# Kernel optimization log

Hardware: AMD Instinct MI355X
Metric: run time of the kernel (lower is better)

The kernel has to match this reference:

```python
import jax, jax.numpy as jnp
import numpy as np

MUL0, MUL1, MUL2, NMOD = 128, 64, 32, 2  # multiplicities of 0e,1e,2e and modalities
D0, D1, D2 = MUL0, MUL1 * 3, MUL2 * 5     # 128, 192, 160 -> total 480


def setup_inputs() -> dict:
    key = jax.random.key(0)
    ks = jax.random.split(key, 7)
    N, G = 200000, 512
    x = jax.random.normal(ks[0], (N, D0 + D1 + D2), dtype=jnp.float32)
    modal_attr = jax.random.uniform(ks[1], (G, NMOD), dtype=jnp.float32)
    W0 = jax.random.normal(ks[2], (MUL0, MUL0), dtype=jnp.float32)
    W0m = jax.random.normal(ks[3], (NMOD, MUL0), dtype=jnp.float32)
    W1 = jax.random.normal(ks[4], (MUL1, MUL1), dtype=jnp.float32)
    W2 = jax.random.normal(ks[5], (MUL2, MUL2), dtype=jnp.float32)
    batch = jnp.sort(jax.random.randint(ks[6], (N,), 0, G, dtype=jnp.int64))
    return {"x": x, "modal_attr": modal_attr, "W0": W0, "W0m": W0m,
            "W1": W1, "W2": W2, "batch": batch}


def reference(x, modal_attr, W0, W0m, W1, W2, batch):
    N = x.shape[0]
    # modality one-hot gathered per node and concatenated (appended 2x0e irrep)
    modal = modal_attr[batch]  # [N, NMOD]
    x0 = x[:, :D0]                                   # [N, 128]  0e
    x1 = x[:, D0:D0 + D1].reshape(N, MUL1, 3)        # [N, 64, 3] 1e
    x2 = x[:, D0 + D1:].reshape(N, MUL2, 5)          # [N, 32, 5] 2e
    # e3nn Linear: per-(l,p) block linear, paths summed, /sqrt(total fan-in mul)
    inv0 = 1.0 / np.sqrt(MUL0 + NMOD).astype(np.float32)
    out0 = (x0 @ W0 + modal @ W0m) * inv0            # [N, 128]
    out1 = jnp.einsum('nim,io->nom', x1, W1) * (1.0 / np.sqrt(MUL1).astype(np.float32))
    out2 = jnp.einsum('nim,io->nom', x2, W2) * (1.0 / np.sqrt(MUL2).astype(np.float32))
    return jnp.concatenate([out0, out1.reshape(N, D1), out2.reshape(N, D2)], axis=1)
```

## Files before the change

kernel.cpp:

```cpp
#include <hip/hip_runtime.h>
#include <hip/hip_bf16.h>


typedef __attribute__((ext_vector_type(8))) short  short8;
typedef __attribute__((ext_vector_type(4))) float  f32x4;

#define NTH 256
#define BR  32

#define W0H 0
#define W0L 16384
#define W1H 32768
#define W1L 36864
#define W2H 40960
#define W2L 41984

__device__ __forceinline__ unsigned bc2(__hip_bfloat162 h) {
    unsigned u; __builtin_memcpy(&u, &h, 4); return u;
}

struct HL4 { uint2 h, l; };

__device__ __forceinline__ HL4 split4(float a, float b, float c, float d) {
    __hip_bfloat162 h01 = __float22bfloat162_rn({a, b});
    __hip_bfloat162 h23 = __float22bfloat162_rn({c, d});
    float ra = a - __low2float(h01),  rb = b - __high2float(h01);
    float rc = c - __low2float(h23),  rd = d - __high2float(h23);
    __hip_bfloat162 l01 = __float22bfloat162_rn({ra, rb});
    __hip_bfloat162 l23 = __float22bfloat162_rn({rc, rd});
    HL4 r;
    r.h = make_uint2(bc2(h01), bc2(h23));
    r.l = make_uint2(bc2(l01), bc2(l23));
    return r;
}

__device__ __forceinline__ void split_w(float v, unsigned short& h, unsigned short& l) {
    __hip_bfloat16 hb = __float2bfloat16(v);
    float r = v - __bfloat162float(hb);
    __hip_bfloat16 lb = __float2bfloat16(r);
    __builtin_memcpy(&h, &hb, 2);
    __builtin_memcpy(&l, &lb, 2);
}

__global__ void prep_weights(const float* __restrict__ W0,
                             const float* __restrict__ W1,
                             const float* __restrict__ W2,
                             unsigned short* __restrict__ ws) {
    const int s0     = blockIdx.x * blockDim.x + threadIdx.x;
    const int STRIDE = gridDim.x * blockDim.x;
    for (int s = s0; s < 16384; s += STRIDE) {
        int j = s & 7, l = (s >> 3) & 63, kt = (s >> 9) & 3, ct = s >> 11;
        int col = ct * 16 + (l & 15);
        int k   = kt * 32 + (l >> 4) * 8 + j;
        unsigned short h, lo;
        split_w(W0[k * 128 + col], h, lo);
        ws[W0H + s] = h; ws[W0L + s] = lo;
    }
    for (int s = s0; s < 4096; s += STRIDE) {
        int j = s & 7, l = (s >> 3) & 63, kt = (s >> 9) & 1, ct = s >> 10;
        int col = ct * 16 + (l & 15);
        int k   = kt * 32 + (l >> 4) * 8 + j;
        unsigned short h, lo;
        split_w(W1[k * 64 + col], h, lo);
        ws[W1H + s] = h; ws[W1L + s] = lo;
    }
    for (int s = s0; s < 1024; s += STRIDE) {
        int j = s & 7, l = (s >> 3) & 63, ct = s >> 9;
        int col = ct * 16 + (l & 15);
        int k   = (l >> 4) * 8 + j;
        unsigned short h, lo;
        split_w(W2[k * 32 + col], h, lo);
        ws[W2H + s] = h; ws[W2L + s] = lo;
    }
}

#define MFMA(a, b, c) __builtin_amdgcn_mfma_f32_16x16x32_bf16((a), (b), (c), 0, 0, 0)

__global__ __launch_bounds__(NTH, 4) void irreps_mfma_kernel(
    const float* __restrict__ x,
    const float* __restrict__ modal_attr,
    const float* __restrict__ W0m,
    const unsigned short* __restrict__ wsf,
    const int*   __restrict__ batch,
    float*       __restrict__ out,
    int N)
{
    __shared__ __align__(16) char ldsb[25088];
    float* ldsf = reinterpret_cast<float*>(ldsb);

    const int tid  = threadIdx.x;
    const int w    = tid >> 6;
    const int l    = tid & 63;
    const int r    = l & 15;
    const int kg   = l >> 4;
    const int rb0  = (w >> 1) * 16;
    const int ch   = w & 1;
    const int row0 = blockIdx.x * BR;
    const int arow = rb0 + r;

    float am0[4], am1[4];
    #pragma unroll
    for (int reg = 0; reg < 4; ++reg) {
        int n  = row0 + rb0 + kg * 4 + reg;
        int nc = n < N ? n : N - 1;
        int g  = batch[nc];
        am0[reg] = modal_attr[2 * g];
        am1[reg] = modal_attr[2 * g + 1];
    }

    const float4* __restrict__ x4 = reinterpret_cast<const float4*>(x);

    {
        const int seg = tid & 15;
        const int rr0 = tid >> 4;
        #pragma unroll
        for (int t2 = 0; t2 < 2; ++t2) {
            int rr = rr0 + 16 * t2;
            int n  = row0 + rr; n = n < N ? n : N - 1;
            const float4* src = &x4[(size_t)n * 120 + seg * 2];
            float4 a = src[0], b = src[1];
            HL4 p = split4(a.x, a.y, a.z, a.w);
            HL4 q = split4(b.x, b.y, b.z, b.w);
            int byte = (rr * 256 + seg * 16) ^ ((rr & 7) << 4);
            *reinterpret_cast<uint4*>(ldsb + byte)        = make_uint4(p.h.x, p.h.y, q.h.x, q.h.y);
            *reinterpret_cast<uint4*>(ldsb + 8192 + byte) = make_uint4(p.l.x, p.l.y, q.l.x, q.l.y);
        }
    }
    __syncthreads();

    {
        const int sw = (arow & 7) << 4;
        short8 ah[4], al[4];
        #pragma unroll
        for (int kt = 0; kt < 4; ++kt) {
            int byte = (arow * 256 + kt * 64 + kg * 16) ^ sw;
            ah[kt] = *reinterpret_cast<const short8*>(ldsb + byte);
            al[kt] = *reinterpret_cast<const short8*>(ldsb + 8192 + byte);
        }
        __syncthreads();

        #pragma unroll
        for (int ci = 0; ci < 4; ++ci) {
            int ct = ch * 4 + ci;
            f32x4 acc = {0.f, 0.f, 0.f, 0.f};
            #pragma unroll
            for (int kt = 0; kt < 4; ++kt) {
                int b = ct * 4 + kt;
                short8 bh = *reinterpret_cast<const short8*>(wsf + W0H + (size_t)(b * 64 + l) * 8);
                short8 bl = *reinterpret_cast<const short8*>(wsf + W0L + (size_t)(b * 64 + l) * 8);
                acc = MFMA(ah[kt], bh, acc);
                acc = MFMA(al[kt], bh, acc);
                acc = MFMA(ah[kt], bl, acc);
            }
            int col = ct * 16 + r;
            float wm0 = W0m[col], wm1 = W0m[128 + col];
            #pragma unroll
            for (int reg = 0; reg < 4; ++reg)
                ldsf[(rb0 + kg * 4 + reg) * 132 + col] =
                    (acc[reg] + am0[reg] * wm0 + am1[reg] * wm1) * 0.08770580193070293f;
        }
    }
    __syncthreads();

    {
        #pragma unroll
        for (int j = 0; j < 4; ++j) {
            int idx = tid + j * NTH;
            int row = idx >> 5, c4 = idx & 31;
            int n   = row0 + row;
            if (n < N)
                *reinterpret_cast<float4*>(out + (size_t)n * 480 + c4 * 4) =
                    *reinterpret_cast<const float4*>(ldsf + row * 132 + c4 * 4);
        }
    }
    __syncthreads();

    {
        const int ig  = tid & 15;
        const int rr0 = tid >> 4;
        #pragma unroll
        for (int t2 = 0; t2 < 2; ++t2) {
            int rr = rr0 + 16 * t2;
            int n  = row0 + rr; n = n < N ? n : N - 1;
            const float4* src = &x4[(size_t)n * 120 + 32 + ig * 3];
            float4 f0 = src[0], f1 = src[1], f2 = src[2];
            HL4 s0 = split4(f0.x, f0.w, f1.z, f2.y);
            HL4 s1 = split4(f0.y, f1.x, f1.w, f2.z);
            HL4 s2 = split4(f0.z, f1.y, f2.x, f2.w);
            int rbyte = (rr * 128 + ig * 8) ^ ((rr & 7) << 4);
            *reinterpret_cast<uint2*>(ldsb + 0 * 4096 + rbyte)         = s0.h;
            *reinterpret_cast<uint2*>(ldsb + 1 * 4096 + rbyte)         = s1.h;
            *reinterpret_cast<uint2*>(ldsb + 2 * 4096 + rbyte)         = s2.h;
            *reinterpret_cast<uint2*>(ldsb + 12288 + 0 * 4096 + rbyte) = s0.l;
            *reinterpret_cast<uint2*>(ldsb + 12288 + 1 * 4096 + rbyte) = s1.l;
            *reinterpret_cast<uint2*>(ldsb + 12288 + 2 * 4096 + rbyte) = s2.l;
        }
    }
    __syncthreads();

    {
        const int sw = (arow & 7) << 4;
        short8 ah1[3][2], al1[3][2];
        #pragma unroll
        for (int m = 0; m < 3; ++m) {
            #pragma unroll
            for (int kt = 0; kt < 2; ++kt) {
                int byte = (arow * 128 + kt * 64 + kg * 16) ^ sw;
                ah1[m][kt] = *reinterpret_cast<const short8*>(ldsb + m * 4096 + byte);
                al1[m][kt] = *reinterpret_cast<const short8*>(ldsb + 12288 + m * 4096 + byte);
            }
        }
        __syncthreads();

        #pragma unroll
        for (int ci = 0; ci < 2; ++ci) {
            int ct = ch * 2 + ci;
            short8 bh[2], bl[2];
            #pragma unroll
            for (int kt = 0; kt < 2; ++kt) {
                int b = ct * 2 + kt;
                bh[kt] = *reinterpret_cast<const short8*>(wsf + W1H + (size_t)(b * 64 + l) * 8);
                bl[kt] = *reinterpret_cast<const short8*>(wsf + W1L + (size_t)(b * 64 + l) * 8);
            }
            #pragma unroll
            for (int m = 0; m < 3; ++m) {
                f32x4 acc = {0.f, 0.f, 0.f, 0.f};
                #pragma unroll
                for (int kt = 0; kt < 2; ++kt) {
                    acc = MFMA(ah1[m][kt], bh[kt], acc);
                    acc = MFMA(al1[m][kt], bh[kt], acc);
                    acc = MFMA(ah1[m][kt], bl[kt], acc);
                }
                int col = 3 * (ct * 16 + r) + m;
                #pragma unroll
                for (int reg = 0; reg < 4; ++reg)
                    ldsf[(rb0 + kg * 4 + reg) * 196 + col] = acc[reg] * 0.125f;
            }
        }
    }
    __syncthreads();

    {
        #pragma unroll
        for (int j = 0; j < 6; ++j) {
            int idx = tid + j * NTH;
            int row = idx / 48, c4 = idx - row * 48;
            int n   = row0 + row;
            if (n < N)
                *reinterpret_cast<float4*>(out + (size_t)n * 480 + 128 + c4 * 4) =
                    *reinterpret_cast<const float4*>(ldsf + row * 196 + c4 * 4);
        }
    }
    __syncthreads();

    {
        int rr = tid >> 3, ig = tid & 7;
        int n  = row0 + rr; n = n < N ? n : N - 1;
        const float4* src = &x4[(size_t)n * 120 + 80 + ig * 5];
        float f[20];
        #pragma unroll
        for (int q = 0; q < 5; ++q) {
            float4 v = src[q];
            f[q * 4 + 0] = v.x; f[q * 4 + 1] = v.y; f[q * 4 + 2] = v.z; f[q * 4 + 3] = v.w;
        }
        int rbyte = (rr * 64 + ig * 8) ^ ((rr & 3) << 4);
        #pragma unroll
        for (int m = 0; m < 5; ++m) {
            HL4 s = split4(f[m], f[5 + m], f[10 + m], f[15 + m]);
            *reinterpret_cast<uint2*>(ldsb + m * 2048 + rbyte)         = s.h;
            *reinterpret_cast<uint2*>(ldsb + 10240 + m * 2048 + rbyte) = s.l;
        }
    }
    __syncthreads();

    {
        const int sw2 = (arow & 3) << 4;
        short8 ah2[5], al2[5];
        #pragma unroll
        for (int m = 0; m < 5; ++m) {
            int byte = (arow * 64 + kg * 16) ^ sw2;
            ah2[m] = *reinterpret_cast<const short8*>(ldsb + m * 2048 + byte);
            al2[m] = *reinterpret_cast<const short8*>(ldsb + 10240 + m * 2048 + byte);
        }
        __syncthreads();

        int ct = ch;
        short8 bh = *reinterpret_cast<const short8*>(wsf + W2H + (size_t)(ct * 64 + l) * 8);
        short8 bl = *reinterpret_cast<const short8*>(wsf + W2L + (size_t)(ct * 64 + l) * 8);
        #pragma unroll
        for (int m = 0; m < 5; ++m) {
            f32x4 acc = {0.f, 0.f, 0.f, 0.f};
            acc = MFMA(ah2[m], bh, acc);
            acc = MFMA(al2[m], bh, acc);
            acc = MFMA(ah2[m], bl, acc);
            int col = 5 * (ct * 16 + r) + m;
            #pragma unroll
            for (int reg = 0; reg < 4; ++reg)
                ldsf[(rb0 + kg * 4 + reg) * 164 + col] = acc[reg] * 0.17677669529663687f;
        }
    }
    __syncthreads();

    {
        #pragma unroll
        for (int j = 0; j < 5; ++j) {
            int idx = tid + j * NTH;
            int row = idx / 40, c4 = idx - row * 40;
            int n   = row0 + row;
            if (n < N)
                *reinterpret_cast<float4*>(out + (size_t)n * 480 + 320 + c4 * 4) =
                    *reinterpret_cast<const float4*>(ldsf + row * 164 + c4 * 4);
        }
    }
}

extern "C" void kernel_launch(void* const* d_in, const int* in_sizes, int n_in,
                              void* d_out, int out_size, void* d_ws, size_t ws_size,
                              hipStream_t stream) {
    const float* x     = (const float*)d_in[0];
    const float* modal = (const float*)d_in[1];
    const float* W0    = (const float*)d_in[2];
    const float* W0m   = (const float*)d_in[3];
    const float* W1    = (const float*)d_in[4];
    const float* W2    = (const float*)d_in[5];
    const int*   batch = (const int*)d_in[6];
    float* out = (float*)d_out;
    unsigned short* ws = (unsigned short*)d_ws;

    const int N = in_sizes[6];

    prep_weights<<<84, NTH, 0, stream>>>(W0, W1, W2, ws);

    const int grid = (N + BR - 1) / BR;
    irreps_mfma_kernel<<<grid, NTH, 0, stream>>>(x, modal, W0m, ws, batch, out, N);
}
```

Baseline: 163.8 us.

## Split fused irreps kernel into three per-irrep kernels with non-aliased LDS

Splits the single kernel that handled the 0e, 1e and 2e blocks one after another into three separate launches, one per irrep block. Each kernel gets its own LDS buffer in which the bf16 staging area and the fp32 output staging area no longer overlap, so the barrier after the fragment loads is removed. The aim is fewer barriers and lighter per-kernel register and LDS use for better occupancy. The cost is two extra launches, and each kernel re-reads its own slice of x with weaker cross-phase overlap.

Measured after the change: 189.4 us. +15.6%, slower.

```diff
diff --git a/kernel.cpp b/kernel.cpp
--- a/kernel.cpp
+++ b/kernel.cpp
@@ -76,7 +76,7 @@
 
 #define MFMA(a, b, c) __builtin_amdgcn_mfma_f32_16x16x32_bf16((a), (b), (c), 0, 0, 0)
 
-__global__ __launch_bounds__(NTH, 4) void irreps_mfma_kernel(
+__global__ __launch_bounds__(NTH, 4) void kA(
     const float* __restrict__ x,
     const float* __restrict__ modal_attr,
     const float* __restrict__ W0m,
@@ -85,8 +85,8 @@
     float*       __restrict__ out,
     int N)
 {
-    __shared__ __align__(16) char ldsb[25088];
-    float* ldsf = reinterpret_cast<float*>(ldsb);
+    __shared__ __align__(16) char ldsb[33280];
+    float* ldsf = reinterpret_cast<float*>(ldsb + 16384);
 
     const int tid  = threadIdx.x;
     const int w    = tid >> 6;
@@ -137,8 +137,6 @@
             ah[kt] = *reinterpret_cast<const short8*>(ldsb + byte);
             al[kt] = *reinterpret_cast<const short8*>(ldsb + 8192 + byte);
         }
-        __syncthreads();
-
         #pragma unroll
         for (int ci = 0; ci < 4; ++ci) {
             int ct = ch * 4 + ci;
@@ -173,7 +171,28 @@
                     *reinterpret_cast<const float4*>(ldsf + row * 132 + c4 * 4);
         }
     }
-    __syncthreads();
+}
+
+__global__ __launch_bounds__(NTH, 3) void kB(
+    const float* __restrict__ x,
+    const unsigned short* __restrict__ wsf,
+    float*       __restrict__ out,
+    int N)
+{
+    __shared__ __align__(16) char ldsb[49664];
+    float* ldsf = reinterpret_cast<float*>(ldsb + 24576);
+
+    const int tid  = threadIdx.x;
+    const int w    = tid >> 6;
+    const int l    = tid & 63;
+    const int r    = l & 15;
+    const int kg   = l >> 4;
+    const int rb0  = (w >> 1) * 16;
+    const int ch   = w & 1;
+    const int row0 = blockIdx.x * BR;
+    const int arow = rb0 + r;
+
+    const float4* __restrict__ x4 = reinterpret_cast<const float4*>(x);
 
     {
         const int ig  = tid & 15;
@@ -210,8 +229,6 @@
                 al1[m][kt] = *reinterpret_cast<const short8*>(ldsb + 12288 + m * 4096 + byte);
             }
         }
-        __syncthreads();
-
         #pragma unroll
         for (int ci = 0; ci < 2; ++ci) {
             int ct = ch * 2 + ci;
@@ -251,7 +268,28 @@
                     *reinterpret_cast<const float4*>(ldsf + row * 196 + c4 * 4);
         }
     }
-    __syncthreads();
+}
+
+__global__ __launch_bounds__(NTH, 3) void kC(
+    const float* __restrict__ x,
+    const unsigned short* __restrict__ wsf,
+    float*       __restrict__ out,
+    int N)
+{
+    __shared__ __align__(16) char ldsb[41472];
+    float* ldsf = reinterpret_cast<float*>(ldsb + 20480);
+
+    const int tid  = threadIdx.x;
+    const int w    = tid >> 6;
+    const int l    = tid & 63;
+    const int r    = l & 15;
+    const int kg   = l >> 4;
+    const int rb0  = (w >> 1) * 16;
+    const int ch   = w & 1;
+    const int row0 = blockIdx.x * BR;
+    const int arow = rb0 + r;
+
+    const float4* __restrict__ x4 = reinterpret_cast<const float4*>(x);
 
     {
         int rr = tid >> 3, ig = tid & 7;
@@ -282,8 +320,6 @@
             ah2[m] = *reinterpret_cast<const short8*>(ldsb + m * 2048 + byte);
             al2[m] = *reinterpret_cast<const short8*>(ldsb + 10240 + m * 2048 + byte);
         }
-        __syncthreads();
-
         int ct = ch;
         short8 bh = *reinterpret_cast<const short8*>(wsf + W2H + (size_t)(ct * 64 + l) * 8);
         short8 bl = *reinterpret_cast<const short8*>(wsf + W2L + (size_t)(ct * 64 + l) * 8);
@@ -327,10 +363,11 @@
     float* out = (float*)d_out;
     unsigned short* ws = (unsigned short*)d_ws;
 
-    const int N = in_sizes[6];
+    const int N    = in_sizes[6];
+    const int grid = (N + BR - 1) / BR;
 
     prep_weights<<<84, NTH, 0, stream>>>(W0, W1, W2, ws);
-
-    const int grid = (N + BR - 1) / BR;
-    irreps_mfma_kernel<<<grid, NTH, 0, stream>>>(x, modal, W0m, ws, batch, out, N);
-}
+    kA<<<grid, NTH, 0, stream>>>(x, modal, W0m, ws, batch, out, N);
+    kB<<<grid, NTH, 0, stream>>>(x, ws, out, N);
+    kC<<<grid, NTH, 0, stream>>>(x, ws, out, N);
+}
```

## Split LDS into input and output regions and prefetch next irrep blocks into registers

Applied to the files above, without the earlier changes.

The shared buffer is split into separate input and output regions so that staging the next irrep's split bf16 operands can overlap with the copy-out of the previous block's results. Global loads for the l=1 and l=2 blocks are issued early into registers, one phase before they are needed, which hides memory latency behind the MFMA work. Several barriers are removed. In exchange, LDS use roughly doubles and the launch-bounds occupancy hint drops from 4 to 3 blocks, and register pressure rises from the prefetched float4s.

After: 159.5 us, median of 2. -2.6%, faster.

```diff
diff --git a/kernel.cpp b/kernel.cpp
--- a/kernel.cpp
+++ b/kernel.cpp
@@ -14,6 +14,9 @@
 #define W1L 36864
 #define W2H 40960
 #define W2L 41984
+
+#define IN0   0
+#define OUT0  24576
 
 __device__ __forceinline__ unsigned bc2(__hip_bfloat162 h) {
     unsigned u; __builtin_memcpy(&u, &h, 4); return u;
@@ -76,7 +79,7 @@
 
 #define MFMA(a, b, c) __builtin_amdgcn_mfma_f32_16x16x32_bf16((a), (b), (c), 0, 0, 0)
 
-__global__ __launch_bounds__(NTH, 4) void irreps_mfma_kernel(
+__global__ __launch_bounds__(NTH, 3) void irreps_mfma_kernel(
     const float* __restrict__ x,
     const float* __restrict__ modal_attr,
     const float* __restrict__ W0m,
@@ -85,8 +88,9 @@
     float*       __restrict__ out,
     int N)
 {
-    __shared__ __align__(16) char ldsb[25088];
-    float* ldsf = reinterpret_cast<float*>(ldsb);
+    __shared__ __align__(16) char ldsb[49664];
+    char*  inb  = ldsb + IN0;
+    float* ldsf = reinterpret_cast<float*>(ldsb + OUT0);
 
     const int tid  = threadIdx.x;
     const int w    = tid >> 6;
@@ -122,8 +126,21 @@
             HL4 p = split4(a.x, a.y, a.z, a.w);
             HL4 q = split4(b.x, b.y, b.z, b.w);
             int byte = (rr * 256 + seg * 16) ^ ((rr & 7) << 4);
-            *reinterpret_cast<uint4*>(ldsb + byte)        = make_uint4(p.h.x, p.h.y, q.h.x, q.h.y);
-            *reinterpret_cast<uint4*>(ldsb + 8192 + byte) = make_uint4(p.l.x, p.l.y, q.l.x, q.l.y);
+            *reinterpret_cast<uint4*>(inb + byte)        = make_uint4(p.h.x, p.h.y, q.h.x, q.h.y);
+            *reinterpret_cast<uint4*>(inb + 8192 + byte) = make_uint4(p.l.x, p.l.y, q.l.x, q.l.y);
+        }
+    }
+
+    float4 bld[2][3];
+    {
+        const int ig  = tid & 15;
+        const int rr0 = tid >> 4;
+        #pragma unroll
+        for (int t2 = 0; t2 < 2; ++t2) {
+            int rr = rr0 + 16 * t2;
+            int n  = row0 + rr; n = n < N ? n : N - 1;
+            const float4* src = &x4[(size_t)n * 120 + 32 + ig * 3];
+            bld[t2][0] = src[0]; bld[t2][1] = src[1]; bld[t2][2] = src[2];
         }
     }
     __syncthreads();
@@ -134,11 +151,9 @@
         #pragma unroll
         for (int kt = 0; kt < 4; ++kt) {
             int byte = (arow * 256 + kt * 64 + kg * 16) ^ sw;
-            ah[kt] = *reinterpret_cast<const short8*>(ldsb + byte);
-            al[kt] = *reinterpret_cast<const short8*>(ldsb + 8192 + byte);
-        }
-        __syncthreads();
-
+            ah[kt] = *reinterpret_cast<const short8*>(inb + byte);
+            al[kt] = *reinterpret_cast<const short8*>(inb + 8192 + byte);
+        }
         #pragma unroll
         for (int ci = 0; ci < 4; ++ci) {
             int ct = ch * 4 + ci;
@@ -163,6 +178,33 @@
     __syncthreads();
 
     {
+        const int ig  = tid & 15;
+        const int rr0 = tid >> 4;
+        #pragma unroll
+        for (int t2 = 0; t2 < 2; ++t2) {
+            int rr = rr0 + 16 * t2;
+            float4 f0 = bld[t2][0], f1 = bld[t2][1], f2 = bld[t2][2];
+            HL4 s0 = split4(f0.x, f0.w, f1.z, f2.y);
+            HL4 s1 = split4(f0.y, f1.x, f1.w, f2.z);
+            HL4 s2 = split4(f0.z, f1.y, f2.x, f2.w);
+            int rbyte = (rr * 128 + ig * 8) ^ ((rr & 7) << 4);
+            *reinterpret_cast<uint2*>(inb + 0 * 4096 + rbyte)         = s0.h;
+            *reinterpret_cast<uint2*>(inb + 1 * 4096 + rbyte)         = s1.h;
+            *reinterpret_cast<uint2*>(inb + 2 * 4096 + rbyte)         = s2.h;
+            *reinterpret_cast<uint2*>(inb + 12288 + 0 * 4096 + rbyte) = s0.l;
+            *reinterpret_cast<uint2*>(inb + 12288 + 1 * 4096 + rbyte) = s1.l;
+            *reinterpret_cast<uint2*>(inb + 12288 + 2 * 4096 + rbyte) = s2.l;
+        }
+    }
+    float4 cld[5];
+    {
+        int rr = tid >> 3, ig = tid & 7;
+        int n  = row0 + rr; n = n < N ? n : N - 1;
+        const float4* src = &x4[(size_t)n * 120 + 80 + ig * 5];
+        #pragma unroll
+        for (int q = 0; q < 5; ++q) cld[q] = src[q];
+    }
+    {
         #pragma unroll
         for (int j = 0; j < 4; ++j) {
             int idx = tid + j * NTH;
@@ -176,29 +218,6 @@
     __syncthreads();
 
     {
-        const int ig  = tid & 15;
-        const int rr0 = tid >> 4;
-        #pragma unroll
-        for (int t2 = 0; t2 < 2; ++t2) {
-            int rr = rr0 + 16 * t2;
-            int n  = row0 + rr; n = n < N ? n : N - 1;
-            const float4* src = &x4[(size_t)n * 120 + 32 + ig * 3];
-            float4 f0 = src[0], f1 = src[1], f2 = src[2];
-            HL4 s0 = split4(f0.x, f0.w, f1.z, f2.y);
-            HL4 s1 = split4(f0.y, f1.x, f1.w, f2.z);
-            HL4 s2 = split4(f0.z, f1.y, f2.x, f2.w);
-            int rbyte = (rr * 128 + ig * 8) ^ ((rr & 7) << 4);
-            *reinterpret_cast<uint2*>(ldsb + 0 * 4096 + rbyte)         = s0.h;
-            *reinterpret_cast<uint2*>(ldsb + 1 * 4096 + rbyte)         = s1.h;
-            *reinterpret_cast<uint2*>(ldsb + 2 * 4096 + rbyte)         = s2.h;
-            *reinterpret_cast<uint2*>(ldsb + 12288 + 0 * 4096 + rbyte) = s0.l;
-            *reinterpret_cast<uint2*>(ldsb + 12288 + 1 * 4096 + rbyte) = s1.l;
-            *reinterpret_cast<uint2*>(ldsb + 12288 + 2 * 4096 + rbyte) = s2.l;
-        }
-    }
-    __syncthreads();
-
-    {
         const int sw = (arow & 7) << 4;
         short8 ah1[3][2], al1[3][2];
         #pragma unroll
@@ -206,12 +225,10 @@
             #pragma unroll
             for (int kt = 0; kt < 2; ++kt) {
                 int byte = (arow * 128 + kt * 64 + kg * 16) ^ sw;
-                ah1[m][kt] = *reinterpret_cast<const short8*>(ldsb + m * 4096 + byte);
-                al1[m][kt] = *reinterpret_cast<const short8*>(ldsb + 12288 + m * 4096 + byte);
+                ah1[m][kt] = *reinterpret_cast<const short8*>(inb + m * 4096 + byte);
+                al1[m][kt] = *reinterpret_cast<const short8*>(inb + 12288 + m * 4096 + byte);
             }
         }
-        __syncthreads();
-
         #pragma unroll
         for (int ci = 0; ci < 2; ++ci) {
             int ct = ch * 2 + ci;
@@ -241,6 +258,22 @@
     __syncthreads();
 
     {
+        int rr = tid >> 3, ig = tid & 7;
+        float f[20];
+        #pragma unroll
+        for (int q = 0; q < 5; ++q) {
+            float4 v = cld[q];
+            f[q * 4 + 0] = v.x; f[q * 4 + 1] = v.y; f[q * 4 + 2] = v.z; f[q * 4 + 3] = v.w;
+        }
+        int rbyte = (rr * 64 + ig * 8) ^ ((rr & 3) << 4);
+        #pragma unroll
+        for (int m = 0; m < 5; ++m) {
+            HL4 s = split4(f[m], f[5 + m], f[10 + m], f[15 + m]);
+            *reinterpret_cast<uint2*>(inb + m * 2048 + rbyte)         = s.h;
+            *reinterpret_cast<uint2*>(inb + 10240 + m * 2048 + rbyte) = s.l;
+        }
+    }
+    {
         #pragma unroll
         for (int j = 0; j < 6; ++j) {
             int idx = tid + j * NTH;
@@ -254,36 +287,14 @@
     __syncthreads();
 
     {
-        int rr = tid >> 3, ig = tid & 7;
-        int n  = row0 + rr; n = n < N ? n : N - 1;
-        const float4* src = &x4[(size_t)n * 120 + 80 + ig * 5];
-        float f[20];
-        #pragma unroll
-        for (int q = 0; q < 5; ++q) {
-            float4 v = src[q];
-            f[q * 4 + 0] = v.x; f[q * 4 + 1] = v.y; f[q * 4 + 2] = v.z; f[q * 4 + 3] = v.w;
-        }
-        int rbyte = (rr * 64 + ig * 8) ^ ((rr & 3) << 4);
-        #pragma unroll
-        for (int m = 0; m < 5; ++m) {
-            HL4 s = split4(f[m], f[5 + m], f[10 + m], f[15 + m]);
-            *reinterpret_cast<uint2*>(ldsb + m * 2048 + rbyte)         = s.h;
-            *reinterpret_cast<uint2*>(ldsb + 10240 + m * 2048 + rbyte) = s.l;
-        }
-    }
-    __syncthreads();
-
-    {
         const int sw2 = (arow & 3) << 4;
         short8 ah2[5], al2[5];
         #pragma unroll
         for (int m = 0; m < 5; ++m) {
             int byte = (arow * 64 + kg * 16) ^ sw2;
-            ah2[m] = *reinterpret_cast<const short8*>(ldsb + m * 2048 + byte);
-            al2[m] = *reinterpret_cast<const short8*>(ldsb + 10240 + m * 2048 + byte);
-        }
-        __syncthreads();
-
+            ah2[m] = *reinterpret_cast<const short8*>(inb + m * 2048 + byte);
+            al2[m] = *reinterpret_cast<const short8*>(inb + 10240 + m * 2048 + byte);
+        }
         int ct = ch;
         short8 bh = *reinterpret_cast<const short8*>(wsf + W2H + (size_t)(ct * 64 + l) * 8);
         short8 bl = *reinterpret_cast<const short8*>(wsf + W2L + (size_t)(ct * 64 + l) * 8);
@@ -327,10 +338,9 @@
     float* out = (float*)d_out;
     unsigned short* ws = (unsigned short*)d_ws;
 
-    const int N = in_sizes[6];
+    const int N    = in_sizes[6];
+    const int grid = (N + BR - 1) / BR;
 
     prep_weights<<<84, NTH, 0, stream>>>(W0, W1, W2, ws);
-
-    const int grid = (N + BR - 1) / BR;
     irreps_mfma_kernel<<<grid, NTH, 0, stream>>>(x, modal, W0m, ws, batch, out, N);
 }
```

## Stream x tiles into LDS via async global_load_lds and overlap with MFMA stages

Applied to the files above, without the earlier changes.

Replaces the register-staged load-split-store of each x segment with direct global-to-LDS DMA (global_load_lds, 16 bytes per lane) into a swizzled raw fp32 buffer. The bf16 hi/lo split now happens when reading A fragments from LDS into registers. The next segment's DMA is issued before the current segment's MFMA and output stores, so loads overlap compute. Fewer barriers are needed, but LDS grows to about 49 KB and the occupancy hint drops from 4 to 3 blocks, which may reduce latency hiding.

Measured after the change: 174.7 us. 1.07x slower.

```diff
diff --git a/kernel.cpp b/kernel.cpp
--- a/kernel.cpp
+++ b/kernel.cpp
@@ -34,12 +34,27 @@
     return r;
 }
 
+__device__ __forceinline__ void packhl(const HL4& p, const HL4& q,
+                                       short8& hi, short8& lo) {
+    uint4 h4 = make_uint4(p.h.x, p.h.y, q.h.x, q.h.y);
+    uint4 l4 = make_uint4(p.l.x, p.l.y, q.l.x, q.l.y);
+    __builtin_memcpy(&hi, &h4, 16);
+    __builtin_memcpy(&lo, &l4, 16);
+}
+
 __device__ __forceinline__ void split_w(float v, unsigned short& h, unsigned short& l) {
     __hip_bfloat16 hb = __float2bfloat16(v);
     float r = v - __bfloat162float(hb);
     __hip_bfloat16 lb = __float2bfloat16(r);
     __builtin_memcpy(&h, &hb, 2);
     __builtin_memcpy(&l, &lb, 2);
+}
+
+__device__ __forceinline__ void dma16(const float* g, char* lds_base) {
+    __builtin_amdgcn_global_load_lds(
+        (const __attribute__((address_space(1))) unsigned int*)g,
+        (__attribute__((address_space(3))) unsigned int*)lds_base,
+        16, 0, 0);
 }
 
 __global__ void prep_weights(const float* __restrict__ W0,
@@ -76,7 +91,7 @@
 
 #define MFMA(a, b, c) __builtin_amdgcn_mfma_f32_16x16x32_bf16((a), (b), (c), 0, 0, 0)
 
-__global__ __launch_bounds__(NTH, 4) void irreps_mfma_kernel(
+__global__ __launch_bounds__(NTH, 3) void irreps_mfma_kernel(
     const float* __restrict__ x,
     const float* __restrict__ modal_attr,
     const float* __restrict__ W0m,
@@ -85,8 +100,9 @@
     float*       __restrict__ out,
     int N)
 {
-    __shared__ __align__(16) char ldsb[25088];
-    float* ldsf = reinterpret_cast<float*>(ldsb);
+    __shared__ __align__(16) char ldsb[49664];
+    char*  raw  = ldsb;
+    float* ldsf = reinterpret_cast<float*>(ldsb + 24576);
 
     const int tid  = threadIdx.x;
     const int w    = tid >> 6;
@@ -97,6 +113,18 @@
     const int ch   = w & 1;
     const int row0 = blockIdx.x * BR;
     const int arow = rb0 + r;
+    const int sw   = (arow & 7) << 4;
+
+    #pragma unroll
+    for (int i = 0; i < 4; ++i) {
+        int c   = w * 4 + i;
+        int o   = c * 1024 + l * 16;
+        int row = o >> 9;
+        int so  = o ^ ((row & 7) << 4);
+        int col = so & 511;
+        int n   = row0 + row; n = n < N ? n : N - 1;
+        dma16(x + (size_t)n * 480 + (col >> 2), raw + c * 1024);
+    }
 
     float am0[4], am1[4];
     #pragma unroll
@@ -107,38 +135,31 @@
         am0[reg] = modal_attr[2 * g];
         am1[reg] = modal_attr[2 * g + 1];
     }
-
-    const float4* __restrict__ x4 = reinterpret_cast<const float4*>(x);
-
-    {
-        const int seg = tid & 15;
-        const int rr0 = tid >> 4;
-        #pragma unroll
-        for (int t2 = 0; t2 < 2; ++t2) {
-            int rr = rr0 + 16 * t2;
-            int n  = row0 + rr; n = n < N ? n : N - 1;
-            const float4* src = &x4[(size_t)n * 120 + seg * 2];
-            float4 a = src[0], b = src[1];
-            HL4 p = split4(a.x, a.y, a.z, a.w);
-            HL4 q = split4(b.x, b.y, b.z, b.w);
-            int byte = (rr * 256 + seg * 16) ^ ((rr & 7) << 4);
-            *reinterpret_cast<uint4*>(ldsb + byte)        = make_uint4(p.h.x, p.h.y, q.h.x, q.h.y);
-            *reinterpret_cast<uint4*>(ldsb + 8192 + byte) = make_uint4(p.l.x, p.l.y, q.l.x, q.l.y);
-        }
-    }
-    __syncthreads();
-
-    {
-        const int sw = (arow & 7) << 4;
-        short8 ah[4], al[4];
-        #pragma unroll
-        for (int kt = 0; kt < 4; ++kt) {
-            int byte = (arow * 256 + kt * 64 + kg * 16) ^ sw;
-            ah[kt] = *reinterpret_cast<const short8*>(ldsb + byte);
-            al[kt] = *reinterpret_cast<const short8*>(ldsb + 8192 + byte);
-        }
-        __syncthreads();
-
+    __syncthreads();
+
+    short8 xah[4], xal[4];
+    #pragma unroll
+    for (int kt = 0; kt < 4; ++kt) {
+        int b0 = arow * 512 + kt * 128 + kg * 32;
+        f32x4 a = *reinterpret_cast<const f32x4*>(raw + (b0 ^ sw));
+        f32x4 b = *reinterpret_cast<const f32x4*>(raw + ((b0 + 16) ^ sw));
+        HL4 p = split4(a[0], a[1], a[2], a[3]);
+        HL4 q = split4(b[0], b[1], b[2], b[3]);
+        packhl(p, q, xah[kt], xal[kt]);
+    }
+    __syncthreads();
+
+    #pragma unroll
+    for (int i = 0; i < 6; ++i) {
+        int c   = w * 6 + i;
+        int o   = c * 1024 + l * 16;
+        int row = o / 768;
+        int so  = o ^ ((row & 7) << 4);
+        int col = so - row * 768;
+        int n   = row0 + row; n = n < N ? n : N - 1;
+        dma16(x + (size_t)n * 480 + 128 + (col >> 2), raw + c * 1024);
+    }
+    {
         #pragma unroll
         for (int ci = 0; ci < 4; ++ci) {
             int ct = ch * 4 + ci;
@@ -148,9 +169,9 @@
                 int b = ct * 4 + kt;
                 short8 bh = *reinterpret_cast<const short8*>(wsf + W0H + (size_t)(b * 64 + l) * 8);
                 short8 bl = *reinterpret_cast<const short8*>(wsf + W0L + (size_t)(b * 64 + l) * 8);
-                acc = MFMA(ah[kt], bh, acc);
-                acc = MFMA(al[kt], bh, acc);
-                acc = MFMA(ah[kt], bl, acc);
+                acc = MFMA(xah[kt], bh, acc);
+                acc = MFMA(xal[kt], bh, acc);
+                acc = MFMA(xah[kt], bl, acc);
             }
             int col = ct * 16 + r;
             float wm0 = W0m[col], wm1 = W0m[128 + col];
@@ -162,6 +183,24 @@
     }
     __syncthreads();
 
+    short8 xbh[3][2], xbl[3][2];
+    #pragma unroll
+    for (int kt = 0; kt < 2; ++kt) {
+        int b0 = arow * 768 + kt * 384 + kg * 96;
+        float f[24];
+        #pragma unroll
+        for (int q = 0; q < 6; ++q) {
+            f32x4 v = *reinterpret_cast<const f32x4*>(raw + ((b0 + q * 16) ^ sw));
+            f[q * 4 + 0] = v[0]; f[q * 4 + 1] = v[1];
+            f[q * 4 + 2] = v[2]; f[q * 4 + 3] = v[3];
+        }
+        #pragma unroll
+        for (int m = 0; m < 3; ++m) {
+            HL4 p = split4(f[0 + m], f[3 + m], f[6 + m],  f[9 + m]);
+            HL4 q = split4(f[12 + m], f[15 + m], f[18 + m], f[21 + m]);
+            packhl(p, q, xbh[m][kt], xbl[m][kt]);
+        }
+    }
     {
         #pragma unroll
         for (int j = 0; j < 4; ++j) {
@@ -175,43 +214,17 @@
     }
     __syncthreads();
 
-    {
-        const int ig  = tid & 15;
-        const int rr0 = tid >> 4;
-        #pragma unroll
-        for (int t2 = 0; t2 < 2; ++t2) {
-            int rr = rr0 + 16 * t2;
-            int n  = row0 + rr; n = n < N ? n : N - 1;
-            const float4* src = &x4[(size_t)n * 120 + 32 + ig * 3];
-            float4 f0 = src[0], f1 = src[1], f2 = src[2];
-            HL4 s0 = split4(f0.x, f0.w, f1.z, f2.y);
-            HL4 s1 = split4(f0.y, f1.x, f1.w, f2.z);
-            HL4 s2 = split4(f0.z, f1.y, f2.x, f2.w);
-            int rbyte = (rr * 128 + ig * 8) ^ ((rr & 7) << 4);
-            *reinterpret_cast<uint2*>(ldsb + 0 * 4096 + rbyte)         = s0.h;
-            *reinterpret_cast<uint2*>(ldsb + 1 * 4096 + rbyte)         = s1.h;
-            *reinterpret_cast<uint2*>(ldsb + 2 * 4096 + rbyte)         = s2.h;
-            *reinterpret_cast<uint2*>(ldsb + 12288 + 0 * 4096 + rbyte) = s0.l;
-            *reinterpret_cast<uint2*>(ldsb + 12288 + 1 * 4096 + rbyte) = s1.l;
-            *reinterpret_cast<uint2*>(ldsb + 12288 + 2 * 4096 + rbyte) = s2.l;
-        }
-    }
-    __syncthreads();
-
-    {
-        const int sw = (arow & 7) << 4;
-        short8 ah1[3][2], al1[3][2];
-        #pragma unroll
-        for (int m = 0; m < 3; ++m) {
-            #pragma unroll
-            for (int kt = 0; kt < 2; ++kt) {
-                int byte = (arow * 128 + kt * 64 + kg * 16) ^ sw;
-                ah1[m][kt] = *reinterpret_cast<const short8*>(ldsb + m * 4096 + byte);
-                al1[m][kt] = *reinterpret_cast<const short8*>(ldsb + 12288 + m * 4096 + byte);
-            }
-        }
-        __syncthreads();
-
+    #pragma unroll
+    for (int i = 0; i < 5; ++i) {
+        int c   = w * 5 + i;
+        int o   = c * 1024 + l * 16;
+        int row = o / 640;
+        int so  = o ^ ((row & 7) << 4);
+        int col = so - row * 640;
+        int n   = row0 + row; n = n < N ? n : N - 1;
+        dma16(x + (size_t)n * 480 + 320 + (col >> 2), raw + c * 1024);
+    }
+    {
         #pragma unroll
         for (int ci = 0; ci < 2; ++ci) {
             int ct = ch * 2 + ci;
@@ -227,9 +240,9 @@
                 f32x4 acc = {0.f, 0.f, 0.f, 0.f};
                 #pragma unroll
                 for (int kt = 0; kt < 2; ++kt) {
-                    acc = MFMA(ah1[m][kt], bh[kt], acc);
-                    acc = MFMA(al1[m][kt], bh[kt], acc);
-                    acc = MFMA(ah1[m][kt], bl[kt], acc);
+                    acc = MFMA(xbh[m][kt], bh[kt], acc);
+                    acc = MFMA(xbl[m][kt], bh[kt], acc);
+                    acc = MFMA(xbh[m][kt], bl[kt], acc);
                 }
                 int col = 3 * (ct * 16 + r) + m;
                 #pragma unroll
@@ -240,6 +253,23 @@
     }
     __syncthreads();
 
+    short8 xch[5], xcl[5];
+    {
+        int b0 = arow * 640 + kg * 160;
+        float f[40];
+        #pragma unroll
+        for (int q = 0; q < 10; ++q) {
+            f32x4 v = *reinterpret_cast<const f32x4*>(raw + ((b0 + q * 16) ^ sw));
+            f[q * 4 + 0] = v[0]; f[q * 4 + 1] = v[1];
+            f[q * 4 + 2] = v[2]; f[q * 4 + 3] = v[3];
+        }
+        #pragma unroll
+        for (int m = 0; m < 5; ++m) {
+            HL4 p = split4(f[0 + m],  f[5 + m],  f[10 + m], f[15 + m]);
+            HL4 q = split4(f[20 + m], f[25 + m], f[30 + m], f[35 + m]);
+            packhl(p, q, xch[m], xcl[m]);
+        }
+    }
     {
         #pragma unroll
         for (int j = 0; j < 6; ++j) {
@@ -254,45 +284,15 @@
     __syncthreads();
 
     {
-        int rr = tid >> 3, ig = tid & 7;
-        int n  = row0 + rr; n = n < N ? n : N - 1;
-        const float4* src = &x4[(size_t)n * 120 + 80 + ig * 5];
-        float f[20];
-        #pragma unroll
-        for (int q = 0; q < 5; ++q) {
-            float4 v = src[q];
-            f[q * 4 + 0] = v.x; f[q * 4 + 1] = v.y; f[q * 4 + 2] = v.z; f[q * 4 + 3] = v.w;
-        }
-        int rbyte = (rr * 64 + ig * 8) ^ ((rr & 3) << 4);
-        #pragma unroll
-        for (int m = 0; m < 5; ++m) {
-            HL4 s = split4(f[m], f[5 + m], f[10 + m], f[15 + m]);
-            *reinterpret_cast<uint2*>(ldsb + m * 2048 + rbyte)         = s.h;
-            *reinterpret_cast<uint2*>(ldsb + 10240 + m * 2048 + rbyte) = s.l;
-        }
-    }
-    __syncthreads();
-
-    {
-        const int sw2 = (arow & 3) << 4;
-        short8 ah2[5], al2[5];
-        #pragma unroll
-        for (int m = 0; m < 5; ++m) {
-            int byte = (arow * 64 + kg * 16) ^ sw2;
-            ah2[m] = *reinterpret_cast<const short8*>(ldsb + m * 2048 + byte);
-            al2[m] = *reinterpret_cast<const short8*>(ldsb + 10240 + m * 2048 + byte);
-        }
-        __syncthreads();
-
         int ct = ch;
         short8 bh = *reinterpret_cast<const short8*>(wsf + W2H + (size_t)(ct * 64 + l) * 8);
         short8 bl = *reinterpret_cast<const short8*>(wsf + W2L + (size_t)(ct * 64 + l) * 8);
         #pragma unroll
         for (int m = 0; m < 5; ++m) {
             f32x4 acc = {0.f, 0.f, 0.f, 0.f};
-            acc = MFMA(ah2[m], bh, acc);
-            acc = MFMA(al2[m], bh, acc);
-            acc = MFMA(ah2[m], bl, acc);
+            acc = MFMA(xch[m], bh, acc);
+            acc = MFMA(xcl[m], bh, acc);
+            acc = MFMA(xch[m], bl, acc);
             int col = 5 * (ct * 16 + r) + m;
             #pragma unroll
             for (int reg = 0; reg < 4; ++reg)
@@ -327,10 +327,9 @@
     float* out = (float*)d_out;
     unsigned short* ws = (unsigned short*)d_ws;
 
-    const int N = in_sizes[6];
+    const int N    = in_sizes[6];
+    const int grid = (N + BR - 1) / BR;
 
     prep_weights<<<84, NTH, 0, stream>>>(W0, W1, W2, ws);
-
-    const int grid = (N + BR - 1) / BR;
     irreps_mfma_kernel<<<grid, NTH, 0, stream>>>(x, modal, W0m, ws, batch, out, N);
 }
```
